# Optimization experiments

Hardware: AMD Instinct MI355X
Metric: run time of the kernel (lower is better)

The kernel has to match this reference:

```python
import jax, jax.numpy as jnp
import numpy as np

N = 8192
FEAT = 3
TRIG = 2
SA = 2
H = 64
ACT = 3
NEG = -1.0e9
EPS = 1e-5


def setup_inputs() -> dict:
    key = jax.random.key(0)
    ks = jax.random.split(key, 24)
    s = 0.05
    node_features = jax.random.uniform(ks[0], (N, FEAT), dtype=jnp.float32)
    adj = jax.random.randint(ks[1], (N, N), 0, 2).astype(jnp.float32)
    # ensure self-loops so every row has at least one neighbor
    adj_matrix = jnp.maximum(adj, jnp.eye(N, dtype=jnp.float32))
    trigger_context = jax.random.uniform(ks[2], (TRIG,), dtype=jnp.float32)
    sa_priors = jax.random.normal(ks[3], (N, SA), dtype=jnp.float32)
    p = lambda k, sh: jax.random.normal(k, sh, dtype=jnp.float32) * s
    return {
        "node_features": node_features,
        "adj_matrix": adj_matrix,
        "trigger_context": trigger_context,
        "sa_priors": sa_priors,
        # node_encoder: Linear(5,64) -> ReLU -> Linear(64,64)
        "w1": p(ks[4], (FEAT + TRIG, H)), "b1": jnp.zeros((H,), jnp.float32),
        "w2": p(ks[5], (H, H)), "b2": jnp.zeros((H,), jnp.float32),
        "wq": p(ks[6], (H, H)), "bq": jnp.zeros((H,), jnp.float32),
        "wk": p(ks[7], (H, H)), "bk": jnp.zeros((H,), jnp.float32),
        "wg": p(ks[8], (TRIG, H)), "bg": jnp.zeros((H,), jnp.float32),
        "stateful_bias": jnp.zeros((1,), jnp.float32),
        "wm": p(ks[9], (H, H)), "bm": jnp.zeros((H,), jnp.float32),
        "ln_g": jnp.ones((H,), jnp.float32), "ln_b": jnp.zeros((H,), jnp.float32),
        "wa1": p(ks[10], (H + SA, H)), "ba1": jnp.zeros((H,), jnp.float32),
        "wa2": p(ks[11], (H, ACT)), "ba2": jnp.zeros((ACT,), jnp.float32),
    }


def reference(node_features, adj_matrix, trigger_context, sa_priors,
              w1, b1, w2, b2, wq, bq, wk, bk, wg, bg, stateful_bias,
              wm, bm, ln_g, ln_b, wa1, ba1, wa2, ba2):
    n = node_features.shape[0]
    trig = jnp.broadcast_to(trigger_context[None, :], (n, TRIG))
    x = jnp.concatenate([node_features, trig], axis=1)          # [N, 5]
    h = jax.nn.relu(x @ w1 + b1) @ w2 + b2                       # [N, H]
    q = h @ wq + bq
    k = h @ wk + bk
    scores = (q @ k.T) * (1.0 / np.sqrt(H))                      # [N, N]
    gate_factor = jnp.mean(jax.nn.sigmoid(trigger_context @ wg + bg))
    topo = jnp.where(adj_matrix == 0, jnp.float32(NEG), adj_matrix)
    is_stateful = node_features[:, 2]
    is_reactive = 1.0 - trigger_context[0]
    sb = jnp.outer(is_stateful, is_stateful) * (stateful_bias[0] * is_reactive)
    scores = scores * gate_factor + topo + sb
    attn = jax.nn.softmax(scores, axis=1)                        # [N, N]
    messages = h @ wm + bm
    aggregated = attn @ messages                                 # [N, H]
    z = h + aggregated
    mu = jnp.mean(z, axis=-1, keepdims=True)
    var = jnp.mean(jnp.square(z - mu), axis=-1, keepdims=True)
    emb = (z - mu) * jax.lax.rsqrt(var + EPS) * ln_g + ln_b      # LayerNorm
    ai = jnp.concatenate([emb, sa_priors], axis=1)               # [N, H+2]
    q_values = jax.nn.relu(ai @ wa1 + ba1) @ wa2 + ba2           # [N, 3]
    return q_values
```

## Files before the change

kernel.cpp:

```cpp
#include <hip/hip_runtime.h>
#include <hip/hip_bf16.h>
#include <math.h>

#define N 8192
#define NEGV -1000000000.0f
#define EPSV 1e-05f
#define NSPLIT 8
#define CPS (N / NSPLIT)
#define NTILE (CPS / 64)

typedef short bf16x8 __attribute__((ext_vector_type(8)));
typedef float f32x4 __attribute__((ext_vector_type(4)));
typedef unsigned short u16;

#define WS_SCAL 0
#define WS_H    64
#define WS_ST   (WS_H + N * 64)
#define WS_SBI  (WS_ST + N)
#define WS_DEN  (WS_SBI + N)
#define WS_AGG  (WS_DEN + NSPLIT * N)
#define WS_F_END (WS_AGG + NSPLIT * N * 64)
#define WU_BASE (WS_F_END * 2)
#define WU_QB (WU_BASE)
#define WU_KF (WU_BASE + N * 64)
#define WU_MB (WU_BASE + 2 * N * 64)
#define WU_MF (WU_BASE + 3 * N * 64)

static __device__ __forceinline__ u16 f2bf(float f) {
    __hip_bfloat16 h = __float2bfloat16(f);
    return *(u16*)&h;
}

__global__ void prep_k(const float* __restrict__ tc, const float* __restrict__ wg,
                       const float* __restrict__ bg, const float* __restrict__ sbias,
                       float* __restrict__ scal) {
    int j = threadIdx.x;
    float v = tc[0] * wg[j] + tc[1] * wg[64 + j] + bg[j];
    float g = 1.0f / (1.0f + __expf(-v));
    for (int off = 32; off; off >>= 1) g += __shfl_xor(g, off, 64);
    if (j == 0) {
        scal[0] = 0.125f * (g * (1.0f / 64.0f));
        scal[1] = sbias[0] * (1.0f - tc[0]);
    }
}

__global__ __launch_bounds__(256) void embed_k(
    const float* __restrict__ nf, const float* __restrict__ tc,
    const float* __restrict__ w1, const float* __restrict__ b1,
    const float* __restrict__ w2, const float* __restrict__ b2,
    const float* __restrict__ wq, const float* __restrict__ bq,
    const float* __restrict__ wk, const float* __restrict__ bk,
    const float* __restrict__ wm, const float* __restrict__ bm,
    float* __restrict__ ws)
{
    const int w = threadIdx.x >> 6, lane = threadIdx.x & 63;
    const int row = blockIdx.x * 4 + w;
    __shared__ float ts[4][64], hs[4][64];
    const float qscale = ws[WS_SCAL + 0];
    const float coef   = ws[WS_SCAL + 1];
    const float f0 = nf[row * 3], f1 = nf[row * 3 + 1], f2 = nf[row * 3 + 2];
    const float t0 = tc[0], t1 = tc[1];
    float v = b1[lane];
    v = fmaf(f0, w1[lane], v);
    v = fmaf(f1, w1[64 + lane], v);
    v = fmaf(f2, w1[128 + lane], v);
    v = fmaf(t0, w1[192 + lane], v);
    v = fmaf(t1, w1[256 + lane], v);
    ts[w][lane] = fmaxf(v, 0.0f);
    __syncthreads();
    float hv = b2[lane];
    #pragma unroll 8
    for (int j = 0; j < 64; j++) hv = fmaf(ts[w][j], w2[j * 64 + lane], hv);
    hs[w][lane] = hv;
    ws[WS_H + row * 64 + lane] = hv;
    __syncthreads();
    float qv = bq[lane], kv = bk[lane], mv = bm[lane];
    #pragma unroll 4
    for (int j = 0; j < 64; j++) {
        const float hj = hs[w][j];
        qv = fmaf(hj, wq[j * 64 + lane], qv);
        kv = fmaf(hj, wk[j * 64 + lane], kv);
        mv = fmaf(hj, wm[j * 64 + lane], mv);
    }
    u16* wu = (u16*)ws;
    wu[WU_QB + row * 64 + lane] = f2bf(qv * qscale);
    {
        const size_t kb4 = row >> 6;
        const int ct = row & 3, n16r = (row & 63) >> 2;
        const int half = lane >> 5, quadl = (lane >> 3) & 3, jl = lane & 7;
        const size_t flat = ((((kb4 * 4 + ct) * 2 + half) * 4 + quadl) * 16 + n16r) * 8 + jl;
        wu[WU_KF + flat] = f2bf(kv);
    }
    wu[WU_MB + row * 64 + lane] = f2bf(mv);
    if (lane == 0) {
        ws[WS_ST + row]  = f2;
        ws[WS_SBI + row] = f2 * coef;
    }
}

__global__ __launch_bounds__(256) void mfrag_k(float* __restrict__ ws) {
    const u16* mb = (const u16*)ws + WU_MB;
    u16* mf = (u16*)ws + WU_MF;
    __shared__ __align__(16) u16 tile[64][72];
    const int jb = blockIdx.x;
    const int t = threadIdx.x;
    {
        const int r = t >> 2, cb = (t & 3) * 16;
        *(uint4*)&tile[r][cb]     = *(const uint4*)&mb[(size_t)(jb * 64 + r) * 64 + cb];
        *(uint4*)&tile[r][cb + 8] = *(const uint4*)&mb[(size_t)(jb * 64 + r) * 64 + cb + 8];
    }
    __syncthreads();
    #pragma unroll
    for (int cc = 0; cc < 2; cc++) {
        const int c = t * 2 + cc;
        const int n16 = c & 15, quad = (c >> 4) & 3;
        const int half = (c >> 6) & 1, nt = c >> 7;
        u16 tmp[8];
        #pragma unroll
        for (int j = 0; j < 8; j++) tmp[j] = tile[half * 32 + quad * 8 + j][nt * 16 + n16];
        *(uint4*)&mf[(size_t)jb * 4096 + (size_t)c * 8] = *(uint4*)&tmp[0];
    }
}

__global__ __launch_bounds__(256, 4) void attn_k(const float* __restrict__ adj,
                                                 float* __restrict__ ws)
{
    const int rb = blockIdx.x, sp = blockIdx.y;
    const int i0 = rb * 64, j0 = sp * CPS;
    const int tid = threadIdx.x;
    const int lane = tid & 63;
    const int quad = lane >> 4, n16 = lane & 15;
    const int m0 = (tid >> 6) * 16;

    __shared__ __align__(16) u16 ps[64][76];

    const u16* qb = (const u16*)ws + WU_QB;
    const u16* kf = (const u16*)ws + WU_KF;
    const u16* mf = (const u16*)ws + WU_MF;
    const float* st_g = ws + WS_ST;

    const bf16x8 aq0 = *(const bf16x8*)&qb[(size_t)(i0 + m0 + n16) * 64 + quad * 8];
    const bf16x8 aq1 = *(const bf16x8*)&qb[(size_t)(i0 + m0 + n16) * 64 + 32 + quad * 8];
    float sbr[4];
    #pragma unroll
    for (int v = 0; v < 4; v++) sbr[v] = ws[WS_SBI + i0 + m0 + quad * 4 + v];

    f32x4 acc[4];
    #pragma unroll
    for (int i = 0; i < 4; i++) acc[i] = (f32x4){0.f, 0.f, 0.f, 0.f};
    float den[4] = {0.f, 0.f, 0.f, 0.f};

    const int fragoff = (quad * 16 + n16) * 8;

    #pragma unroll 2
    for (int t = 0; t < NTILE; t++) {
        const int jt = j0 + t * 64;
        const u16* kfb = kf + (size_t)(jt >> 6) * 4096;
        const u16* mfb = mf + (size_t)(jt >> 6) * 4096;

        float4 aa[4];
        #pragma unroll
        for (int reg = 0; reg < 4; reg++)
            aa[reg] = *(const float4*)&adj[(size_t)(i0 + m0 + quad * 4 + reg) * N + jt + n16 * 4];
        const float4 st4 = *(const float4*)&st_g[jt + n16 * 4];

        f32x4 s[4];
        #pragma unroll
        for (int ct = 0; ct < 4; ct++) {
            const bf16x8 b0 = *(const bf16x8*)&kfb[(ct * 2 + 0) * 512 + fragoff];
            const bf16x8 b1 = *(const bf16x8*)&kfb[(ct * 2 + 1) * 512 + fragoff];
            f32x4 sv = {0.f, 0.f, 0.f, 0.f};
            sv = __builtin_amdgcn_mfma_f32_16x16x32_bf16(aq0, b0, sv, 0, 0, 0);
            sv = __builtin_amdgcn_mfma_f32_16x16x32_bf16(aq1, b1, sv, 0, 0, 0);
            s[ct] = sv;
        }

        #pragma unroll
        for (int reg = 0; reg < 4; reg++) {
            const float sb_r = sbr[reg];
            float a0 = aa[reg].x, a1 = aa[reg].y, a2 = aa[reg].z, a3 = aa[reg].w;
            const float p0 = __expf(s[0][reg] + (a0 == 0.0f ? NEGV : a0) + sb_r * st4.x);
            const float p1 = __expf(s[1][reg] + (a1 == 0.0f ? NEGV : a1) + sb_r * st4.y);
            const float p2 = __expf(s[2][reg] + (a2 == 0.0f ? NEGV : a2) + sb_r * st4.z);
            const float p3 = __expf(s[3][reg] + (a3 == 0.0f ? NEGV : a3) + sb_r * st4.w);
            den[reg] += (p0 + p1) + (p2 + p3);
            ushort4 pw;
            pw.x = f2bf(p0); pw.y = f2bf(p1); pw.z = f2bf(p2); pw.w = f2bf(p3);
            *(ushort4*)&ps[m0 + quad * 4 + reg][n16 * 4] = pw;
        }

        const bf16x8 ap0 = *(const bf16x8*)&ps[m0 + n16][quad * 8];
        const bf16x8 ap1 = *(const bf16x8*)&ps[m0 + n16][32 + quad * 8];
        #pragma unroll
        for (int nt = 0; nt < 4; nt++) {
            const bf16x8 b0 = *(const bf16x8*)&mfb[(nt * 2 + 0) * 512 + fragoff];
            const bf16x8 b1 = *(const bf16x8*)&mfb[(nt * 2 + 1) * 512 + fragoff];
            acc[nt] = __builtin_amdgcn_mfma_f32_16x16x32_bf16(ap0, b0, acc[nt], 0, 0, 0);
            acc[nt] = __builtin_amdgcn_mfma_f32_16x16x32_bf16(ap1, b1, acc[nt], 0, 0, 0);
        }
    }

    float* aggp = ws + WS_AGG + (size_t)sp * N * 64;
    #pragma unroll
    for (int nt = 0; nt < 4; nt++) {
        #pragma unroll
        for (int reg = 0; reg < 4; reg++) {
            aggp[(size_t)(i0 + m0 + quad * 4 + reg) * 64 + nt * 16 + n16] = acc[nt][reg];
        }
    }
    #pragma unroll
    for (int reg = 0; reg < 4; reg++) {
        float d = den[reg];
        d += __shfl_xor(d, 1, 64);
        d += __shfl_xor(d, 2, 64);
        d += __shfl_xor(d, 4, 64);
        d += __shfl_xor(d, 8, 64);
        if (n16 == 0) ws[WS_DEN + sp * N + i0 + m0 + quad * 4 + reg] = d;
    }
}

__global__ __launch_bounds__(256) void final_k(
    const float* __restrict__ sa, const float* __restrict__ ln_g,
    const float* __restrict__ ln_b,
    const float* __restrict__ wa1, const float* __restrict__ ba1,
    const float* __restrict__ wa2, const float* __restrict__ ba2,
    const float* __restrict__ ws, float* __restrict__ out)
{
    const int w = threadIdx.x >> 6, lane = threadIdx.x & 63;
    const int row = blockIdx.x * 4 + w;
    __shared__ float es[4][64], hs2[4][64];
    float a = 0.0f;
    #pragma unroll
    for (int sp = 0; sp < NSPLIT; sp++)
        a += ws[WS_AGG + (size_t)sp * N * 64 + (size_t)row * 64 + lane];
    float d = 0.0f;
    #pragma unroll
    for (int sp = 0; sp < NSPLIT; sp++) d += ws[WS_DEN + sp * N + row];
    const float z = ws[WS_H + row * 64 + lane] + a / d;
    float mu = z;
    for (int off = 32; off; off >>= 1) mu += __shfl_xor(mu, off, 64);
    mu *= (1.0f / 64.0f);
    const float zc = z - mu;
    float var = zc * zc;
    for (int off = 32; off; off >>= 1) var += __shfl_xor(var, off, 64);
    var *= (1.0f / 64.0f);
    const float emb = zc * rsqrtf(var + EPSV) * ln_g[lane] + ln_b[lane];
    es[w][lane] = emb;
    __syncthreads();
    const float sa0 = sa[row * 2], sa1 = sa[row * 2 + 1];
    float hv = ba1[lane];
    #pragma unroll 8
    for (int c = 0; c < 64; c++) hv = fmaf(es[w][c], wa1[c * 64 + lane], hv);
    hv = fmaf(sa0, wa1[64 * 64 + lane], hv);
    hv = fmaf(sa1, wa1[65 * 64 + lane], hv);
    hs2[w][lane] = fmaxf(hv, 0.0f);
    __syncthreads();
    if (lane < 3) {
        float o = ba2[lane];
        for (int u = 0; u < 64; u++) o = fmaf(hs2[w][u], wa2[u * 3 + lane], o);
        out[row * 3 + lane] = o;
    }
}

extern "C" void kernel_launch(void* const* d_in, const int* in_sizes, int n_in,
                              void* d_out, int out_size, void* d_ws, size_t ws_size,
                              hipStream_t stream)
{
    const float* nf  = (const float*)d_in[0];
    const float* adj = (const float*)d_in[1];
    const float* tc  = (const float*)d_in[2];
    const float* sa  = (const float*)d_in[3];
    const float* w1  = (const float*)d_in[4];
    const float* b1  = (const float*)d_in[5];
    const float* w2  = (const float*)d_in[6];
    const float* b2  = (const float*)d_in[7];
    const float* wq  = (const float*)d_in[8];
    const float* bq  = (const float*)d_in[9];
    const float* wk  = (const float*)d_in[10];
    const float* bk  = (const float*)d_in[11];
    const float* wg  = (const float*)d_in[12];
    const float* bg  = (const float*)d_in[13];
    const float* sb  = (const float*)d_in[14];
    const float* wm  = (const float*)d_in[15];
    const float* bm  = (const float*)d_in[16];
    const float* lng = (const float*)d_in[17];
    const float* lnb = (const float*)d_in[18];
    const float* wa1 = (const float*)d_in[19];
    const float* ba1 = (const float*)d_in[20];
    const float* wa2 = (const float*)d_in[21];
    const float* ba2 = (const float*)d_in[22];
    float* ws  = (float*)d_ws;
    float* out = (float*)d_out;

    prep_k<<<1, 64, 0, stream>>>(tc, wg, bg, sb, ws + WS_SCAL);
    embed_k<<<N / 4, 256, 0, stream>>>(nf, tc, w1, b1, w2, b2, wq, bq, wk, bk,
                                       wm, bm, ws);
    mfrag_k<<<N / 64, 256, 0, stream>>>(ws);
    attn_k<<<dim3(N / 64, NSPLIT), 256, 0, stream>>>(adj, ws);
    final_k<<<N / 4, 256, 0, stream>>>(sa, lng, lnb, wa1, ba1, wa2, ba2, ws, out);
}
```

Baseline: 502.5 us.

## Prefetch next adjacency tile with nontemporal loads and double the column split

The attention kernel now loads the adjacency and stateful values for the next 64-column tile before computing the current one, a software prefetch meant to hide global-memory latency on the 256 MB adjacency stream. Adjacency loads and partial-aggregate stores use nontemporal hints so streaming data bypasses cache retention. NSPLIT goes from 8 to 16, doubling the grid's parallelism but also the partial aggregate and denominator buffers the final kernel must reduce. The extra live registers from prefetching may reduce occupancy.

```diff
diff --git a/kernel.cpp b/kernel.cpp
--- a/kernel.cpp
+++ b/kernel.cpp
@@ -5,7 +5,7 @@
 #define N 8192
 #define NEGV -1000000000.0f
 #define EPSV 1e-05f
-#define NSPLIT 8
+#define NSPLIT 16
 #define CPS (N / NSPLIT)
 #define NTILE (CPS / 64)
 
@@ -29,6 +29,9 @@
 static __device__ __forceinline__ u16 f2bf(float f) {
     __hip_bfloat16 h = __float2bfloat16(f);
     return *(u16*)&h;
+}
+static __device__ __forceinline__ f32x4 ntload4(const float* p) {
+    return __builtin_nontemporal_load((const f32x4*)p);
 }
 
 __global__ void prep_k(const float* __restrict__ tc, const float* __restrict__ wg,
@@ -151,18 +154,29 @@
     float den[4] = {0.f, 0.f, 0.f, 0.f};
 
     const int fragoff = (quad * 16 + n16) * 8;
+    const size_t arow0 = (size_t)(i0 + m0 + quad * 4 + 0) * N + n16 * 4;
+    const size_t arow1 = (size_t)(i0 + m0 + quad * 4 + 1) * N + n16 * 4;
+    const size_t arow2 = (size_t)(i0 + m0 + quad * 4 + 2) * N + n16 * 4;
+    const size_t arow3 = (size_t)(i0 + m0 + quad * 4 + 3) * N + n16 * 4;
+
+    f32x4 aaC0 = ntload4(&adj[arow0 + j0]);
+    f32x4 aaC1 = ntload4(&adj[arow1 + j0]);
+    f32x4 aaC2 = ntload4(&adj[arow2 + j0]);
+    f32x4 aaC3 = ntload4(&adj[arow3 + j0]);
+    f32x4 stC  = *(const f32x4*)&st_g[j0 + n16 * 4];
 
     #pragma unroll 2
     for (int t = 0; t < NTILE; t++) {
         const int jt = j0 + t * 64;
+        const int jn = j0 + ((t + 1 < NTILE) ? (t + 1) : t) * 64;
         const u16* kfb = kf + (size_t)(jt >> 6) * 4096;
         const u16* mfb = mf + (size_t)(jt >> 6) * 4096;
 
-        float4 aa[4];
-        #pragma unroll
-        for (int reg = 0; reg < 4; reg++)
-            aa[reg] = *(const float4*)&adj[(size_t)(i0 + m0 + quad * 4 + reg) * N + jt + n16 * 4];
-        const float4 st4 = *(const float4*)&st_g[jt + n16 * 4];
+        const f32x4 aaN0 = ntload4(&adj[arow0 + jn]);
+        const f32x4 aaN1 = ntload4(&adj[arow1 + jn]);
+        const f32x4 aaN2 = ntload4(&adj[arow2 + jn]);
+        const f32x4 aaN3 = ntload4(&adj[arow3 + jn]);
+        const f32x4 stN  = *(const f32x4*)&st_g[jn + n16 * 4];
 
         f32x4 s[4];
         #pragma unroll
@@ -175,18 +189,41 @@
             s[ct] = sv;
         }
 
-        #pragma unroll
-        for (int reg = 0; reg < 4; reg++) {
-            const float sb_r = sbr[reg];
-            float a0 = aa[reg].x, a1 = aa[reg].y, a2 = aa[reg].z, a3 = aa[reg].w;
-            const float p0 = __expf(s[0][reg] + (a0 == 0.0f ? NEGV : a0) + sb_r * st4.x);
-            const float p1 = __expf(s[1][reg] + (a1 == 0.0f ? NEGV : a1) + sb_r * st4.y);
-            const float p2 = __expf(s[2][reg] + (a2 == 0.0f ? NEGV : a2) + sb_r * st4.z);
-            const float p3 = __expf(s[3][reg] + (a3 == 0.0f ? NEGV : a3) + sb_r * st4.w);
-            den[reg] += (p0 + p1) + (p2 + p3);
-            ushort4 pw;
-            pw.x = f2bf(p0); pw.y = f2bf(p1); pw.z = f2bf(p2); pw.w = f2bf(p3);
-            *(ushort4*)&ps[m0 + quad * 4 + reg][n16 * 4] = pw;
+        {
+            const float p00 = __expf(s[0][0] + (aaC0.x == 0.0f ? NEGV : aaC0.x) + sbr[0] * stC.x);
+            const float p01 = __expf(s[1][0] + (aaC0.y == 0.0f ? NEGV : aaC0.y) + sbr[0] * stC.y);
+            const float p02 = __expf(s[2][0] + (aaC0.z == 0.0f ? NEGV : aaC0.z) + sbr[0] * stC.z);
+            const float p03 = __expf(s[3][0] + (aaC0.w == 0.0f ? NEGV : aaC0.w) + sbr[0] * stC.w);
+            den[0] += (p00 + p01) + (p02 + p03);
+            ushort4 pw; pw.x = f2bf(p00); pw.y = f2bf(p01); pw.z = f2bf(p02); pw.w = f2bf(p03);
+            *(ushort4*)&ps[m0 + quad * 4 + 0][n16 * 4] = pw;
+        }
+        {
+            const float p10 = __expf(s[0][1] + (aaC1.x == 0.0f ? NEGV : aaC1.x) + sbr[1] * stC.x);
+            const float p11 = __expf(s[1][1] + (aaC1.y == 0.0f ? NEGV : aaC1.y) + sbr[1] * stC.y);
+            const float p12 = __expf(s[2][1] + (aaC1.z == 0.0f ? NEGV : aaC1.z) + sbr[1] * stC.z);
+            const float p13 = __expf(s[3][1] + (aaC1.w == 0.0f ? NEGV : aaC1.w) + sbr[1] * stC.w);
+            den[1] += (p10 + p11) + (p12 + p13);
+            ushort4 pw; pw.x = f2bf(p10); pw.y = f2bf(p11); pw.z = f2bf(p12); pw.w = f2bf(p13);
+            *(ushort4*)&ps[m0 + quad * 4 + 1][n16 * 4] = pw;
+        }
+        {
+            const float p20 = __expf(s[0][2] + (aaC2.x == 0.0f ? NEGV : aaC2.x) + sbr[2] * stC.x);
+            const float p21 = __expf(s[1][2] + (aaC2.y == 0.0f ? NEGV : aaC2.y) + sbr[2] * stC.y);
+            const float p22 = __expf(s[2][2] + (aaC2.z == 0.0f ? NEGV : aaC2.z) + sbr[2] * stC.z);
+            const float p23 = __expf(s[3][2] + (aaC2.w == 0.0f ? NEGV : aaC2.w) + sbr[2] * stC.w);
+            den[2] += (p20 + p21) + (p22 + p23);
+            ushort4 pw; pw.x = f2bf(p20); pw.y = f2bf(p21); pw.z = f2bf(p22); pw.w = f2bf(p23);
+            *(ushort4*)&ps[m0 + quad * 4 + 2][n16 * 4] = pw;
+        }
+        {
+            const float p30 = __expf(s[0][3] + (aaC3.x == 0.0f ? NEGV : aaC3.x) + sbr[3] * stC.x);
+            const float p31 = __expf(s[1][3] + (aaC3.y == 0.0f ? NEGV : aaC3.y) + sbr[3] * stC.y);
+            const float p32 = __expf(s[2][3] + (aaC3.z == 0.0f ? NEGV : aaC3.z) + sbr[3] * stC.z);
+            const float p33 = __expf(s[3][3] + (aaC3.w == 0.0f ? NEGV : aaC3.w) + sbr[3] * stC.w);
+            den[3] += (p30 + p31) + (p32 + p33);
+            ushort4 pw; pw.x = f2bf(p30); pw.y = f2bf(p31); pw.z = f2bf(p32); pw.w = f2bf(p33);
+            *(ushort4*)&ps[m0 + quad * 4 + 3][n16 * 4] = pw;
         }
 
         const bf16x8 ap0 = *(const bf16x8*)&ps[m0 + n16][quad * 8];
@@ -198,6 +235,8 @@
             acc[nt] = __builtin_amdgcn_mfma_f32_16x16x32_bf16(ap0, b0, acc[nt], 0, 0, 0);
             acc[nt] = __builtin_amdgcn_mfma_f32_16x16x32_bf16(ap1, b1, acc[nt], 0, 0, 0);
         }
+
+        aaC0 = aaN0; aaC1 = aaN1; aaC2 = aaN2; aaC3 = aaN3; stC = stN;
     }
 
     float* aggp = ws + WS_AGG + (size_t)sp * N * 64;
@@ -205,7 +244,8 @@
     for (int nt = 0; nt < 4; nt++) {
         #pragma unroll
         for (int reg = 0; reg < 4; reg++) {
-            aggp[(size_t)(i0 + m0 + quad * 4 + reg) * 64 + nt * 16 + n16] = acc[nt][reg];
+            __builtin_nontemporal_store(acc[nt][reg],
+                &aggp[(size_t)(i0 + m0 + quad * 4 + reg) * 64 + nt * 16 + n16]);
         }
     }
     #pragma unroll
```

Result: faster. 487.5 us (-3.0%).
